# Optimization experiments

Measured on AMD Instinct MI355X. Metric: run time of the kernel, lower is better.

## Reference

```python
import jax, jax.numpy as jnp
import numpy as np

N = 100000      # nodes
E = 400000      # edges
G = 4096        # graphs in batch
ATOM_DIM = 101
BOND_DIM = 11
D = 128         # latent_dim
L = 3           # num_atom_layers
BN_EPS = 1e-5


def setup_inputs() -> dict:
    key = jax.random.key(0)
    ks = jax.random.split(key, 16)
    x = jax.random.normal(ks[0], (N, ATOM_DIM), dtype=jnp.float32)
    edge_index = jax.random.randint(ks[1], (2, E), 0, N, dtype=jnp.int64)
    batch = jnp.sort(jax.random.randint(ks[2], (N,), 0, G, dtype=jnp.int64))
    edge_attr = jax.random.normal(ks[3], (E, BOND_DIM), dtype=jnp.float32)
    s = 0.05
    embW = jax.random.normal(ks[4], (ATOM_DIM, D), dtype=jnp.float32) * s
    embB = jnp.zeros((D,), dtype=jnp.float32)
    bondW = jax.random.normal(ks[5], (L, BOND_DIM, D), dtype=jnp.float32) * s
    bondB = jnp.zeros((L, D), dtype=jnp.float32)
    W1 = jax.random.normal(ks[6], (L, D, 2 * D), dtype=jnp.float32) * s
    b1 = jnp.zeros((L, 2 * D), dtype=jnp.float32)
    g1 = jnp.ones((L, 2 * D), dtype=jnp.float32)
    be1 = jnp.zeros((L, 2 * D), dtype=jnp.float32)
    W2 = jax.random.normal(ks[7], (L, 2 * D, D), dtype=jnp.float32) * s
    b2 = jnp.zeros((L, D), dtype=jnp.float32)
    gout = jnp.ones((L, D), dtype=jnp.float32)
    bout = jnp.zeros((L, D), dtype=jnp.float32)
    return dict(x=x, edge_attr=edge_attr, embW=embW, embB=embB,
                bondW=bondW, bondB=bondB, W1=W1, b1=b1, g1=g1, be1=be1,
                W2=W2, b2=b2, gout=gout, bout=bout,
                edge_index=edge_index, batch=batch)


def _bn(h, gamma, beta):
    # BatchNorm1d in training mode: batch stats over node axis, biased variance
    m = h.mean(axis=0)
    v = h.var(axis=0)
    return (h - m) * jax.lax.rsqrt(v + BN_EPS) * gamma + beta


def reference(x, edge_attr, embW, embB, bondW, bondB, W1, b1, g1, be1,
              W2, b2, gout, bout, edge_index, batch):
    src, dst = edge_index[0], edge_index[1]
    h = x @ embW + embB                              # [N, D]
    for i in range(L):
        e = edge_attr @ bondW[i] + bondB[i]          # [E, D] bond embedding
        msg = jax.nn.relu(h[src] + e)                # gather + add + relu
        agg = jax.ops.segment_sum(msg, dst, num_segments=N)  # scatter-add
        z = h + agg                                  # (1 + eps) * x + agg, eps = 0
        z = jax.nn.relu(_bn(z @ W1[i] + b1[i], g1[i], be1[i]))  # [N, 2D]
        h = z @ W2[i] + b2[i]                        # [N, D]
        h = _bn(h, gout[i], bout[i])
        if i != L - 1:
            h = jax.nn.relu(h)
    # global mean pool per graph
    sums = jax.ops.segment_sum(h, batch, num_segments=G)            # [G, D]
    cnts = jax.ops.segment_sum(jnp.ones((h.shape[0],), h.dtype), batch,
                               num_segments=G)
    return sums / jnp.maximum(cnts, 1.0)[:, None]
```

## Files before the change

kernel.cpp:

```cpp
#include <hip/hip_runtime.h>
#include <hip/hip_bf16.h>

#define NN 100000
#define EE 400000
#define GG 4096
#define DD 128
#define ATOM_DIM 101
#define BOND_DIM 11
#define EAP 12
#define GEMM_GRID 512

typedef __attribute__((ext_vector_type(8))) short bf16x8;
typedef __attribute__((ext_vector_type(4))) float f32x4;
typedef __attribute__((ext_vector_type(2))) float f32x2;

__device__ __forceinline__ float b2f(short s) {
    unsigned u = ((unsigned)(unsigned short)s) << 16;
    float f; __builtin_memcpy(&f, &u, 4); return f;
}
__device__ __forceinline__ unsigned short f2b(float f) {
    unsigned u; __builtin_memcpy(&u, &f, 4);
    u += 0x7FFFu + ((u >> 16) & 1u);
    return (unsigned short)(u >> 16);
}

__global__ void detect64_kernel(const void* ei, int npairs, int* flag) {
    __shared__ int any;
    if (threadIdx.x == 0) any = 0;
    __syncthreads();
    const int* p = (const int*)ei;
    int v = 0;
    for (int i = threadIdx.x; i < npairs; i += blockDim.x) v |= p[2 * i + 1];
    if (v) atomicOr(&any, 1);
    __syncthreads();
    if (threadIdx.x == 0) *flag = (any == 0) ? 1 : 0;
}
__device__ __forceinline__ int getIdx(const void* p, long i, int is64) {
    if (is64) return (int)(((const long long*)p)[i]);
    return ((const int*)p)[i];
}

__global__ __launch_bounds__(256) void hist_kernel(
    const void* __restrict__ eidx, const int* __restrict__ flag, int* __restrict__ counts) {
    int e = blockIdx.x * 256 + threadIdx.x;
    if (e >= EE) return;
    int is64 = *flag;
    int dn = getIdx(eidx, (long)EE + e, is64);
    atomicAdd(&counts[dn], 1);
}

__global__ __launch_bounds__(256) void scan1_kernel(
    const int* __restrict__ counts, int* __restrict__ tmp, int* __restrict__ bsum, int n) {
    __shared__ int sd[256];
    const int tid = threadIdx.x;
    int i = blockIdx.x * 256 + tid;
    int v = (i < n) ? counts[i] : 0;
    sd[tid] = v; __syncthreads();
    #pragma unroll
    for (int off = 1; off < 256; off <<= 1) {
        int a = (tid >= off) ? sd[tid - off] : 0;
        __syncthreads();
        sd[tid] += a;
        __syncthreads();
    }
    if (i < n) tmp[i] = sd[tid] - v;
    if (tid == 255) bsum[blockIdx.x] = sd[255];
}

__global__ __launch_bounds__(512) void scan2_kernel(
    const int* __restrict__ bsum, int* __restrict__ bsumx, int nb) {
    __shared__ int sd[512];
    const int tid = threadIdx.x;
    int v = (tid < nb) ? bsum[tid] : 0;
    sd[tid] = v; __syncthreads();
    #pragma unroll
    for (int off = 1; off < 512; off <<= 1) {
        int a = (tid >= off) ? sd[tid - off] : 0;
        __syncthreads();
        sd[tid] += a;
        __syncthreads();
    }
    if (tid < nb) bsumx[tid] = sd[tid] - v;
}

__global__ __launch_bounds__(256) void scan3_kernel(
    const int* __restrict__ tmp, const int* __restrict__ bsumx,
    int* __restrict__ row_ptr, int n) {
    int i = blockIdx.x * 256 + threadIdx.x;
    if (i < n) row_ptr[i] = tmp[i] + bsumx[blockIdx.x];
    if (i == 0) row_ptr[n] = EE;
}

__global__ __launch_bounds__(256) void scatter_kernel(
    const void* __restrict__ eidx, const int* __restrict__ flag,
    const float* __restrict__ ea, const int* __restrict__ row_ptr,
    int* __restrict__ cursor, int* __restrict__ src_sorted, float* __restrict__ eas) {
    int e = blockIdx.x * 256 + threadIdx.x;
    if (e >= EE) return;
    int is64 = *flag;
    int dn = getIdx(eidx, (long)EE + e, is64);
    int sv = getIdx(eidx, e, is64);
    int pos = row_ptr[dn] + atomicAdd(&cursor[dn], 1);
    src_sorted[pos] = sv;
    const float* sp = ea + (long)e * BOND_DIM;
    float* dp = eas + (long)pos * EAP;
    #pragma unroll
    for (int k = 0; k < BOND_DIM; ++k) dp[k] = sp[k];
    dp[11] = 0.f;
}

#define EDGE_MATH(TV, EVp, A0, A1)                                              \
    {                                                                           \
        float c0 = bbv.x, c1 = bbv.y;                                           \
        _Pragma("unroll")                                                       \
        for (int k = 0; k < BOND_DIM; ++k) {                                    \
            c0 = fmaf((EVp)[k], wk0[k], c0);                                    \
            c1 = fmaf((EVp)[k], wk1[k], c1);                                    \
        }                                                                       \
        float f0 = b2f((short)((TV) & 0xffff)), f1 = b2f((short)((TV) >> 16));  \
        if (aff) { f0 = fmaxf(f0 * sc0 + sh0, 0.f); f1 = fmaxf(f1 * sc1v + sh1v, 0.f); } \
        A0 += fmaxf(f0 + c0, 0.f);                                              \
        A1 += fmaxf(f1 + c1, 0.f);                                              \
    }

__global__ __launch_bounds__(256) void msg_csr_kernel(
    const unsigned short* __restrict__ h,
    const float* __restrict__ sc, const float* __restrict__ sh,
    const int* __restrict__ src_sorted, const int* __restrict__ row_ptr,
    const float* __restrict__ eas,
    const float* __restrict__ bw,
    const float* __restrict__ bb,
    unsigned short* __restrict__ sout)
{
    const int tid = threadIdx.x;
    const int wave = tid >> 6, lane = tid & 63;
    const int d0 = lane * 2;
    float wk0[BOND_DIM], wk1[BOND_DIM];
    #pragma unroll
    for (int k = 0; k < BOND_DIM; ++k) {
        f32x2 wv = *(const f32x2*)(bw + k * DD + d0);
        wk0[k] = wv.x; wk1[k] = wv.y;
    }
    f32x2 bbv = *(const f32x2*)(bb + d0);
    const bool aff = (sc != nullptr);
    float sc0 = 1.f, sc1v = 1.f, sh0 = 0.f, sh1v = 0.f;
    if (aff) { sc0 = sc[d0]; sc1v = sc[d0 + 1]; sh0 = sh[d0]; sh1v = sh[d0 + 1]; }

    for (int n0 = blockIdx.x * 4 + wave; n0 < NN; n0 += gridDim.x * 4) {
        const int n = __builtin_amdgcn_readfirstlane(n0);
        const int e0 = __builtin_amdgcn_readfirstlane(row_ptr[n]);
        const int e1 = __builtin_amdgcn_readfirstlane(row_ptr[n + 1]);
        float a0 = 0.f, a1 = 0.f;
        int e = e0;
        for (; e + 4 <= e1; e += 4) {
            const int eu = __builtin_amdgcn_readfirstlane(e);
            int sv0 = __builtin_amdgcn_readfirstlane(src_sorted[eu]);
            int sv1 = __builtin_amdgcn_readfirstlane(src_sorted[eu + 1]);
            int sv2 = __builtin_amdgcn_readfirstlane(src_sorted[eu + 2]);
            int sv3 = __builtin_amdgcn_readfirstlane(src_sorted[eu + 3]);
            unsigned tv0 = *(const unsigned*)(h + (long)sv0 * DD + d0);
            unsigned tv1 = *(const unsigned*)(h + (long)sv1 * DD + d0);
            unsigned tv2 = *(const unsigned*)(h + (long)sv2 * DD + d0);
            unsigned tv3 = *(const unsigned*)(h + (long)sv3 * DD + d0);
            const float* ep0 = eas + (long)eu * EAP;
            EDGE_MATH(tv0, ep0, a0, a1)
            EDGE_MATH(tv1, ep0 + EAP, a0, a1)
            EDGE_MATH(tv2, ep0 + 2 * EAP, a0, a1)
            EDGE_MATH(tv3, ep0 + 3 * EAP, a0, a1)
        }
        if (e + 2 <= e1) {
            const int eu = __builtin_amdgcn_readfirstlane(e);
            int sv0 = __builtin_amdgcn_readfirstlane(src_sorted[eu]);
            int sv1 = __builtin_amdgcn_readfirstlane(src_sorted[eu + 1]);
            unsigned tv0 = *(const unsigned*)(h + (long)sv0 * DD + d0);
            unsigned tv1 = *(const unsigned*)(h + (long)sv1 * DD + d0);
            const float* ep0 = eas + (long)eu * EAP;
            EDGE_MATH(tv0, ep0, a0, a1)
            EDGE_MATH(tv1, ep0 + EAP, a0, a1)
            e += 2;
        }
        if (e < e1) {
            const int eu = __builtin_amdgcn_readfirstlane(e);
            int sv = __builtin_amdgcn_readfirstlane(src_sorted[eu]);
            unsigned tv = *(const unsigned*)(h + (long)sv * DD + d0);
            const float* ep0 = eas + (long)eu * EAP;
            EDGE_MATH(tv, ep0, a0, a1)
        }
        unsigned tn = *(const unsigned*)(h + (long)n * DD + d0);
        float t0 = b2f((short)(tn & 0xffff)), t1 = b2f((short)(tn >> 16));
        if (aff) {
            t0 = fmaxf(t0 * sc0 + sh0, 0.f); t1 = fmaxf(t1 * sc1v + sh1v, 0.f);
        }
        unsigned pk = (unsigned)f2b(t0 + a0) | ((unsigned)f2b(t1 + a1) << 16);
        *(unsigned*)(sout + (long)n * DD + d0) = pk;
    }
}

__global__ void pack_w(const float* __restrict__ W, unsigned short* __restrict__ Wf,
                       int Kact, int N, int KSTEPS) {
    int idx = blockIdx.x * blockDim.x + threadIdx.x;
    int NF = N >> 4;
    int total = KSTEPS * NF * 64;
    if (idx >= total) return;
    int l = idx & 63;
    int f = (idx >> 6) % NF;
    int ks = idx / (64 * NF);
    int col = f * 16 + (l & 15);
    int k0 = ks * 32 + (l >> 4) * 8;
    bf16x8 v;
    #pragma unroll
    for (int j = 0; j < 8; ++j) {
        int k = k0 + j;
        v[j] = (k < Kact) ? (short)f2b(W[(long)k * N + col]) : (short)0;
    }
    *(bf16x8*)(Wf + (long)idx * 8) = v;
}

template<int MODE, int KSTEPS, int KACT>
__device__ __forceinline__ void loadA(const void* Ap, long rc, int kg, bf16x8* dst) {
    if (MODE == 1) {
        const float* ap = (const float*)Ap + rc * KACT;
        #pragma unroll
        for (int ks = 0; ks < KSTEPS; ++ks) {
            bf16x8 a;
            #pragma unroll
            for (int j = 0; j < 8; ++j) {
                int gk = ks * 32 + kg + j;
                a[j] = (gk < KACT) ? (short)f2b(ap[gk]) : (short)0;
            }
            dst[ks] = a;
        }
    } else {
        const unsigned short* ap = (const unsigned short*)Ap + rc * (KSTEPS * 32) + kg;
        #pragma unroll
        for (int ks = 0; ks < KSTEPS; ++ks) dst[ks] = *(const bf16x8*)(ap + ks * 32);
    }
}

template<int NF, int KSTEPS, int NHALVES, int MODE, bool OUT_BF16, bool STATS, int KACT = 0>
__global__ __launch_bounds__(256, 2) void gemm_reg(
    const void* __restrict__ Ap,
    const float* __restrict__ sc, const float* __restrict__ sh,
    const unsigned short* __restrict__ Wf,
    const float* __restrict__ bias,
    void* __restrict__ outp,
    float* __restrict__ partial,
    int M)
{
    constexpr int K = KSTEPS * 32;
    constexpr int NCb = NF * 16;
    constexpr int NFtot = NF * NHALVES;
    constexpr int NCtot = NCb * NHALVES;
    constexpr int ESZ = OUT_BF16 ? 2 : 4;
    constexpr int RSTRIDE = NCb + (OUT_BF16 ? 8 : 4);
    constexpr int ROWBYTES = NCb * ESZ;
    constexpr int CHUNKS = 64 * ROWBYTES / 16;
    constexpr int CPR = ROWBYTES / 16;

    __shared__ __align__(16) char sOut[2][64 * RSTRIDE * ESZ];
    __shared__ float s_sc[(MODE == 2) ? K : 1];
    __shared__ float s_sh[(MODE == 2) ? K : 1];
    __shared__ float s_ps[STATS ? 2 * NCb : 1];

    const int tid = threadIdx.x;
    const int wave = tid >> 6, l = tid & 63;
    const int kg = (l >> 4) * 8;

    int half, mt;
    if (NHALVES == 2) {
        int b = blockIdx.x;
        half = (b >> 3) & 1;
        mt = (b & 7) | ((b >> 4) << 3);
    } else {
        half = 0; mt = blockIdx.x;
    }
    const int col0 = half * NCb;
    const int bstep = gridDim.x / NHALVES;

    if (MODE == 2 || STATS) {
        if (MODE == 2) {
            for (int i = tid; i < K; i += 256) { s_sc[i] = sc[i]; s_sh[i] = sh[i]; }
        }
        if (STATS) {
            for (int i = tid; i < 2 * NCb; i += 256) s_ps[i] = 0.f;
        }
        __syncthreads();
    }

    bf16x8 bfr[KSTEPS][NF];
    {
        const bf16x8* wp = (const bf16x8*)Wf;
        #pragma unroll
        for (int ks = 0; ks < KSTEPS; ++ks)
            #pragma unroll
            for (int f = 0; f < NF; ++f)
                bfr[ks][f] = wp[((long)ks * NFtot + half * NF + f) * 64 + l];
    }

    float bb[NF];
    #pragma unroll
    for (int f = 0; f < NF; ++f) bb[f] = bias[col0 + f * 16 + (l & 15)];

    float ssum[NF], ssq[NF];
    #pragma unroll
    for (int f = 0; f < NF; ++f) { ssum[f] = 0.f; ssq[f] = 0.f; }

    const int MT = (M + 63) >> 6;

    bf16x8 ldA[KSTEPS], ldB[KSTEPS];
    {
        int rr = mt * 64 + wave * 16 + (l & 15);
        int rc = rr < M ? rr : M - 1;
        loadA<MODE, KSTEPS, KACT>(Ap, rc, kg, ldA);
    }

    int pbuf = 0;
    for (; mt < MT; mt += bstep) {
        const int nxt = mt + bstep;
        if (nxt < MT) {
            int rr = nxt * 64 + wave * 16 + (l & 15);
            int rc = rr < M ? rr : M - 1;
            loadA<MODE, KSTEPS, KACT>(Ap, rc, kg, ldB);
        }

        if (MODE == 2) {
            #pragma unroll
            for (int ks = 0; ks < KSTEPS; ++ks) {
                f32x4 s0 = *(const f32x4*)&s_sc[ks * 32 + kg];
                f32x4 s1 = *(const f32x4*)&s_sc[ks * 32 + kg + 4];
                f32x4 h0 = *(const f32x4*)&s_sh[ks * 32 + kg];
                f32x4 h1 = *(const f32x4*)&s_sh[ks * 32 + kg + 4];
                float sv[8] = {s0.x, s0.y, s0.z, s0.w, s1.x, s1.y, s1.z, s1.w};
                float hv[8] = {h0.x, h0.y, h0.z, h0.w, h1.x, h1.y, h1.z, h1.w};
                #pragma unroll
                for (int j = 0; j < 8; ++j) {
                    float v = fmaxf(b2f(ldA[ks][j]) * sv[j] + hv[j], 0.f);
                    ldA[ks][j] = (short)f2b(v);
                }
            }
        }

        f32x4 acc[NF];
        #pragma unroll
        for (int f = 0; f < NF; ++f) acc[f] = (f32x4){0.f, 0.f, 0.f, 0.f};
        #pragma unroll
        for (int ks = 0; ks < KSTEPS; ++ks)
            #pragma unroll
            for (int f = 0; f < NF; ++f)
                acc[f] = __builtin_amdgcn_mfma_f32_16x16x32_bf16(ldA[ks], bfr[ks][f], acc[f], 0, 0, 0);

        const int rtile = mt * 64;
        char* sb = sOut[pbuf];
        #pragma unroll
        for (int f = 0; f < NF; ++f) {
            const int cl = f * 16 + (l & 15);
            #pragma unroll
            for (int j = 0; j < 4; ++j) {
                const int rl = wave * 16 + (l >> 4) * 4 + j;
                float v = acc[f][j] + bb[f];
                if (OUT_BF16) ((unsigned short*)sb)[rl * RSTRIDE + cl] = f2b(v);
                else          ((float*)sb)[rl * RSTRIDE + cl] = v;
                if (STATS && rtile + rl < M) { ssum[f] += v; ssq[f] += v * v; }
            }
        }
        __syncthreads();

        const int rmax = M - rtile;
        #pragma unroll
        for (int i = 0; i < CHUNKS / 256; ++i) {
            int c = i * 256 + tid;
            int row = c / CPR;
            int off = (c % CPR) * 16;
            if (row < rmax) {
                f32x4 v = *(const f32x4*)(sb + row * (RSTRIDE * ESZ) + off);
                char* gp = (char*)outp + ((long)(rtile + row) * NCtot + col0) * ESZ + off;
                *(f32x4*)gp = v;
            }
        }
        pbuf ^= 1;

        #pragma unroll
        for (int ks = 0; ks < KSTEPS; ++ks) ldA[ks] = ldB[ks];
    }

    if (STATS) {
        #pragma unroll
        for (int f = 0; f < NF; ++f) {
            float s = ssum[f], q = ssq[f];
            s += __shfl_xor(s, 16); s += __shfl_xor(s, 32);
            q += __shfl_xor(q, 16); q += __shfl_xor(q, 32);
            if (l < 16) {
                atomicAdd(&s_ps[f * 16 + l], s);
                atomicAdd(&s_ps[NCb + f * 16 + l], q);
            }
        }
        __syncthreads();
        float* pb = partial + (long)blockIdx.x * 2 * NCb;
        for (int i = tid; i < 2 * NCb; i += 256) pb[i] = s_ps[i];
    }
}

__global__ __launch_bounds__(64) void bn_finalize_p(
    const float* __restrict__ partial, int nblk, int ncb, int halves,
    const float* __restrict__ gamma, const float* __restrict__ beta,
    float invN, float* __restrict__ sc, float* __restrict__ sh)
{
    const int c = blockIdx.x;
    const int t = threadIdx.x;
    float s = 0.f, q = 0.f;
    for (int b = t; b < nblk; b += 64) {
        int half = (halves == 2) ? ((b >> 3) & 1) : 0;
        if (c / ncb != half) continue;
        const float* pb = partial + (long)b * 2 * ncb;
        s += pb[c % ncb];
        q += pb[ncb + c % ncb];
    }
    #pragma unroll
    for (int off = 1; off < 64; off <<= 1) {
        s += __shfl_xor(s, off);
        q += __shfl_xor(q, off);
    }
    if (t == 0) {
        float m = s * invN;
        float v = q * invN - m * m;
        float g = gamma[c] * rsqrtf(v + 1e-5f);
        sc[c] = g;
        sh[c] = beta[c] - m * g;
    }
}

__global__ __launch_bounds__(64) void pool_kernel(
    const unsigned short* __restrict__ h,
    const float* __restrict__ sc, const float* __restrict__ sh,
    const void* __restrict__ batchp, const int* __restrict__ flag,
    int Nn, float* __restrict__ out)
{
    const int g = blockIdx.x;
    const int t = threadIdx.x;
    const int d0 = t * 2;
    const int is64 = *flag;
    int lo = 0, hi = Nn;
    while (lo < hi) { int mid = (lo + hi) >> 1; if (getIdx(batchp, mid, is64) < g) lo = mid + 1; else hi = mid; }
    const int s0 = lo;
    hi = Nn;
    while (lo < hi) { int mid = (lo + hi) >> 1; if (getIdx(batchp, mid, is64) < g + 1) lo = mid + 1; else hi = mid; }
    const int s1 = lo;
    float a0 = 0.f, a1 = 0.f;
    for (int r = s0; r < s1; ++r) {
        unsigned v = *(const unsigned*)(h + (long)r * DD + d0);
        a0 += b2f((short)(v & 0xffff));
        a1 += b2f((short)(v >> 16));
    }
    const int cnt = s1 - s0;
    f32x2 o; o.x = 0.f; o.y = 0.f;
    if (cnt > 0) {
        float inv = 1.f / (float)cnt;
        o.x = a0 * inv * sc[d0] + sh[d0];
        o.y = a1 * inv * sc[d0 + 1] + sh[d0 + 1];
    }
    *(f32x2*)(out + (long)g * DD + d0) = o;
}

extern "C" void kernel_launch(void* const* d_in, const int* in_sizes, int n_in,
                              void* d_out, int out_size, void* d_ws, size_t ws_size,
                              hipStream_t stream)
{
    const float* x     = (const float*)d_in[0];
    const float* ea    = (const float*)d_in[1];
    const float* embW  = (const float*)d_in[2];
    const float* embB  = (const float*)d_in[3];
    const float* bondW = (const float*)d_in[4];
    const float* bondB = (const float*)d_in[5];
    const float* W1    = (const float*)d_in[6];
    const float* b1    = (const float*)d_in[7];
    const float* g1    = (const float*)d_in[8];
    const float* be1   = (const float*)d_in[9];
    const float* W2    = (const float*)d_in[10];
    const float* b2    = (const float*)d_in[11];
    const float* gout  = (const float*)d_in[12];
    const float* bout  = (const float*)d_in[13];
    const void*  eidx  = d_in[14];
    const void*  batch = d_in[15];
    float* out = (float*)d_out;

    char* w = (char*)d_ws;
    unsigned short* h   = (unsigned short*)w;   w += (long)NN * DD * 2;
    unsigned short* s   = (unsigned short*)w;   w += (long)NN * DD * 2;
    unsigned short* z1  = (unsigned short*)w;   w += (long)NN * 256 * 2;
    float* eas  = (float*)w;                    w += (long)EE * EAP * 4;
    int* src_sorted = (int*)w;                  w += (long)EE * 4;
    int* row_ptr    = (int*)w;                  w += (long)(NN + 1) * 4;
    int* counts     = (int*)w;                  w += (long)NN * 4;
    int* tmp        = (int*)w;                  w += (long)NN * 4;
    int* bsum       = (int*)w;                  w += 1024 * 4;
    int* bsumx      = (int*)w;                  w += 1024 * 4;
    float* partial  = (float*)w;                w += (long)GEMM_GRID * 512 * 4;
    float* sc1  = (float*)w;                    w += 256 * 4;
    float* sh1  = (float*)w;                    w += 256 * 4;
    float* sc2  = (float*)w;                    w += 128 * 4;
    float* sh2  = (float*)w;                    w += 128 * 4;
    unsigned short* embWf = (unsigned short*)w; w += 4 * 8  * 64 * 8 * 2;
    unsigned short* W1f   = (unsigned short*)w; w += 3L * 4 * 16 * 64 * 8 * 2;
    unsigned short* W2f   = (unsigned short*)w; w += 3L * 8 * 8  * 64 * 8 * 2;
    int* flag = (int*)w;

    detect64_kernel<<<1, 256, 0, stream>>>(eidx, 256, flag);

    pack_w<<<8, 256, 0, stream>>>(embW, embWf, ATOM_DIM, 128, 4);
    for (int i = 0; i < 3; ++i) {
        pack_w<<<16, 256, 0, stream>>>(W1 + (long)i * 128 * 256, W1f + (long)i * 4 * 16 * 64 * 8, 128, 256, 4);
        pack_w<<<16, 256, 0, stream>>>(W2 + (long)i * 256 * 128, W2f + (long)i * 8 * 8 * 64 * 8, 256, 128, 8);
    }

    const int eblocks = (EE + 255) / 256;
    const int nb = (NN + 255) / 256;
    hipMemsetAsync(counts, 0, (size_t)NN * 4, stream);
    hist_kernel<<<eblocks, 256, 0, stream>>>(eidx, flag, counts);
    scan1_kernel<<<nb, 256, 0, stream>>>(counts, tmp, bsum, NN);
    scan2_kernel<<<1, 512, 0, stream>>>(bsum, bsumx, nb);
    scan3_kernel<<<nb, 256, 0, stream>>>(tmp, bsumx, row_ptr, NN);
    hipMemsetAsync(counts, 0, (size_t)NN * 4, stream);
    scatter_kernel<<<eblocks, 256, 0, stream>>>(eidx, flag, ea, row_ptr, counts, src_sorted, eas);

    gemm_reg<8, 4, 1, 1, true, false, ATOM_DIM><<<GEMM_GRID, 256, 0, stream>>>(
        x, nullptr, nullptr, embWf, embB, h, nullptr, NN);

    const float* scin = nullptr;
    const float* shin = nullptr;

    for (int i = 0; i < 3; ++i) {
        msg_csr_kernel<<<4096, 256, 0, stream>>>(
            h, scin, shin, src_sorted, row_ptr, eas,
            bondW + (long)i * BOND_DIM * DD, bondB + (long)i * DD, s);

        gemm_reg<8, 4, 2, 0, true, true><<<GEMM_GRID, 256, 0, stream>>>(
            s, nullptr, nullptr, W1f + (long)i * 4 * 16 * 64 * 8,
            b1 + (long)i * 256, z1, partial, NN);
        bn_finalize_p<<<256, 64, 0, stream>>>(partial, GEMM_GRID, 128, 2,
            g1 + (long)i * 256, be1 + (long)i * 256, 1.f / NN, sc1, sh1);

        gemm_reg<4, 8, 2, 2, true, true><<<GEMM_GRID, 256, 0, stream>>>(
            z1, sc1, sh1, W2f + (long)i * 8 * 8 * 64 * 8,
            b2 + (long)i * DD, h, partial, NN);
        bn_finalize_p<<<128, 64, 0, stream>>>(partial, GEMM_GRID, 64, 2,
            gout + (long)i * DD, bout + (long)i * DD, 1.f / NN, sc2, sh2);

        scin = sc2; shin = sh2;
    }

    pool_kernel<<<GG, 64, 0, stream>>>(h, sc2, sh2, batch, flag, NN, out);
}
```

Baseline: 451.0 us.

## Fuse BN finalize into GEMM via last-block reduction and merge weight packing

Removes the separate bn_finalize_p launches by having the last GEMM block to finish (tracked with an atomic counter) reduce the per-block partial sums and write the BN scale and shift. All weight packing is merged into one pack_all kernel, and the two counter memsets become one by giving the scatter its own cursor array. This saves several kernel launches and their gaps. The cost is a serial tail where one block reads every partial, plus a dependence on a done counter that must reset itself between launches.

New measurement: 699.6 us. +55.1%, slower.

```diff
diff --git a/kernel.cpp b/kernel.cpp
--- a/kernel.cpp
+++ b/kernel.cpp
@@ -196,15 +196,27 @@
     }
 }
 
-__global__ void pack_w(const float* __restrict__ W, unsigned short* __restrict__ Wf,
-                       int Kact, int N, int KSTEPS) {
-    int idx = blockIdx.x * blockDim.x + threadIdx.x;
+__global__ __launch_bounds__(256) void pack_all(
+    const float* __restrict__ embW, const float* __restrict__ W1, const float* __restrict__ W2,
+    unsigned short* __restrict__ embWf, unsigned short* __restrict__ W1f, unsigned short* __restrict__ W2f)
+{
+    int idx = blockIdx.x * 256 + threadIdx.x;
+    const float* W; unsigned short* Wf; int Kact, N, base;
+    if (idx < 2048) {
+        W = embW; Wf = embWf; Kact = ATOM_DIM; N = 128; base = idx;
+    } else if (idx < 2048 + 3 * 4096) {
+        int r = idx - 2048; int i = r / 4096; base = r % 4096;
+        W = W1 + (long)i * 128 * 256; Wf = W1f + (long)i * 4096 * 8;
+        Kact = 128; N = 256;
+    } else if (idx < 2048 + 6 * 4096) {
+        int r = idx - 2048 - 3 * 4096; int i = r / 4096; base = r % 4096;
+        W = W2 + (long)i * 256 * 128; Wf = W2f + (long)i * 4096 * 8;
+        Kact = 256; N = 128;
+    } else return;
+    int l = base & 63;
     int NF = N >> 4;
-    int total = KSTEPS * NF * 64;
-    if (idx >= total) return;
-    int l = idx & 63;
-    int f = (idx >> 6) % NF;
-    int ks = idx / (64 * NF);
+    int f = (base >> 6) % NF;
+    int ks = base / (64 * NF);
     int col = f * 16 + (l & 15);
     int k0 = ks * 32 + (l >> 4) * 8;
     bf16x8 v;
@@ -213,7 +225,7 @@
         int k = k0 + j;
         v[j] = (k < Kact) ? (short)f2b(W[(long)k * N + col]) : (short)0;
     }
-    *(bf16x8*)(Wf + (long)idx * 8) = v;
+    *(bf16x8*)(Wf + (long)base * 8) = v;
 }
 
 template<int MODE, int KSTEPS, int KACT>
@@ -245,6 +257,9 @@
     const float* __restrict__ bias,
     void* __restrict__ outp,
     float* __restrict__ partial,
+    const float* __restrict__ gamma, const float* __restrict__ beta,
+    float* __restrict__ sc_out, float* __restrict__ sh_out,
+    int* __restrict__ done,
     int M)
 {
     constexpr int K = KSTEPS * 32;
@@ -261,6 +276,7 @@
     __shared__ float s_sc[(MODE == 2) ? K : 1];
     __shared__ float s_sh[(MODE == 2) ? K : 1];
     __shared__ float s_ps[STATS ? 2 * NCb : 1];
+    __shared__ int amLast;
 
     const int tid = threadIdx.x;
     const int wave = tid >> 6, l = tid & 63;
@@ -396,36 +412,37 @@
         }
         __syncthreads();
         float* pb = partial + (long)blockIdx.x * 2 * NCb;
-        for (int i = tid; i < 2 * NCb; i += 256) pb[i] = s_ps[i];
-    }
-}
-
-__global__ __launch_bounds__(64) void bn_finalize_p(
-    const float* __restrict__ partial, int nblk, int ncb, int halves,
-    const float* __restrict__ gamma, const float* __restrict__ beta,
-    float invN, float* __restrict__ sc, float* __restrict__ sh)
-{
-    const int c = blockIdx.x;
-    const int t = threadIdx.x;
-    float s = 0.f, q = 0.f;
-    for (int b = t; b < nblk; b += 64) {
-        int half = (halves == 2) ? ((b >> 3) & 1) : 0;
-        if (c / ncb != half) continue;
-        const float* pb = partial + (long)b * 2 * ncb;
-        s += pb[c % ncb];
-        q += pb[ncb + c % ncb];
-    }
-    #pragma unroll
-    for (int off = 1; off < 64; off <<= 1) {
-        s += __shfl_xor(s, off);
-        q += __shfl_xor(q, off);
-    }
-    if (t == 0) {
-        float m = s * invN;
-        float v = q * invN - m * m;
-        float g = gamma[c] * rsqrtf(v + 1e-5f);
-        sc[c] = g;
-        sh[c] = beta[c] - m * g;
+        for (int i = tid; i < 2 * NCb; i += 256)
+            __hip_atomic_store(&pb[i], s_ps[i], __ATOMIC_RELAXED, __HIP_MEMORY_SCOPE_AGENT);
+        __threadfence();
+        __syncthreads();
+        if (tid == 0) {
+            int prev = atomicAdd(done, 1);
+            amLast = (prev == (int)gridDim.x - 1);
+        }
+        __syncthreads();
+        if (amLast) {
+            __threadfence();
+            const float invN = 1.f / (float)M;
+            for (int c = tid; c < NCtot; c += 256) {
+                const int hh = c / NCb, cl = c % NCb;
+                float s = 0.f, q = 0.f;
+                const int nrel = (NHALVES == 2) ? (GEMM_GRID / 2) : GEMM_GRID;
+                #pragma unroll 8
+                for (int j = 0; j < nrel; ++j) {
+                    int b = (NHALVES == 2) ? (((j >> 3) << 4) | (hh << 3) | (j & 7)) : j;
+                    const float* pb2 = partial + (long)b * 2 * NCb;
+                    s += __hip_atomic_load(&pb2[cl], __ATOMIC_RELAXED, __HIP_MEMORY_SCOPE_AGENT);
+                    q += __hip_atomic_load(&pb2[NCb + cl], __ATOMIC_RELAXED, __HIP_MEMORY_SCOPE_AGENT);
+                }
+                float m = s * invN;
+                float v = q * invN - m * m;
+                float g = gamma[c] * rsqrtf(v + 1e-5f);
+                sc_out[c] = g;
+                sh_out[c] = beta[c] - m * g;
+            }
+            if (tid == 0) *done = 0;
+        }
     }
 }
 
@@ -491,6 +508,8 @@
     int* src_sorted = (int*)w;                  w += (long)EE * 4;
     int* row_ptr    = (int*)w;                  w += (long)(NN + 1) * 4;
     int* counts     = (int*)w;                  w += (long)NN * 4;
+    int* cursor     = (int*)w;                  w += (long)NN * 4;
+    int* done       = (int*)w;                  w += 16 * 4;
     int* tmp        = (int*)w;                  w += (long)NN * 4;
     int* bsum       = (int*)w;                  w += 1024 * 4;
     int* bsumx      = (int*)w;                  w += 1024 * 4;
@@ -504,26 +523,22 @@
     unsigned short* W2f   = (unsigned short*)w; w += 3L * 8 * 8  * 64 * 8 * 2;
     int* flag = (int*)w;
 
+    hipMemsetAsync(counts, 0, ((size_t)2 * NN + 16) * 4, stream);
+
     detect64_kernel<<<1, 256, 0, stream>>>(eidx, 256, flag);
-
-    pack_w<<<8, 256, 0, stream>>>(embW, embWf, ATOM_DIM, 128, 4);
-    for (int i = 0; i < 3; ++i) {
-        pack_w<<<16, 256, 0, stream>>>(W1 + (long)i * 128 * 256, W1f + (long)i * 4 * 16 * 64 * 8, 128, 256, 4);
-        pack_w<<<16, 256, 0, stream>>>(W2 + (long)i * 256 * 128, W2f + (long)i * 8 * 8 * 64 * 8, 256, 128, 8);
-    }
+    pack_all<<<(2048 + 6 * 4096 + 255) / 256, 256, 0, stream>>>(embW, W1, W2, embWf, W1f, W2f);
 
     const int eblocks = (EE + 255) / 256;
     const int nb = (NN + 255) / 256;
-    hipMemsetAsync(counts, 0, (size_t)NN * 4, stream);
     hist_kernel<<<eblocks, 256, 0, stream>>>(eidx, flag, counts);
     scan1_kernel<<<nb, 256, 0, stream>>>(counts, tmp, bsum, NN);
     scan2_kernel<<<1, 512, 0, stream>>>(bsum, bsumx, nb);
     scan3_kernel<<<nb, 256, 0, stream>>>(tmp, bsumx, row_ptr, NN);
-    hipMemsetAsync(counts, 0, (size_t)NN * 4, stream);
-    scatter_kernel<<<eblocks, 256, 0, stream>>>(eidx, flag, ea, row_ptr, counts, src_sorted, eas);
+    scatter_kernel<<<eblocks, 256, 0, stream>>>(eidx, flag, ea, row_ptr, cursor, src_sorted, eas);
 
     gemm_reg<8, 4, 1, 1, true, false, ATOM_DIM><<<GEMM_GRID, 256, 0, stream>>>(
-        x, nullptr, nullptr, embWf, embB, h, nullptr, NN);
+        x, nullptr, nullptr, embWf, embB, h, nullptr,
+        nullptr, nullptr, nullptr, nullptr, nullptr, NN);
 
     const float* scin = nullptr;
     const float* shin = nullptr;
@@ -535,15 +550,13 @@
 
         gemm_reg<8, 4, 2, 0, true, true><<<GEMM_GRID, 256, 0, stream>>>(
             s, nullptr, nullptr, W1f + (long)i * 4 * 16 * 64 * 8,
-            b1 + (long)i * 256, z1, partial, NN);
-        bn_finalize_p<<<256, 64, 0, stream>>>(partial, GEMM_GRID, 128, 2,
-            g1 + (long)i * 256, be1 + (long)i * 256, 1.f / NN, sc1, sh1);
+            b1 + (long)i * 256, z1, partial,
+            g1 + (long)i * 256, be1 + (long)i * 256, sc1, sh1, done, NN);
 
         gemm_reg<4, 8, 2, 2, true, true><<<GEMM_GRID, 256, 0, stream>>>(
             z1, sc1, sh1, W2f + (long)i * 8 * 8 * 64 * 8,
-            b2 + (long)i * DD, h, partial, NN);
-        bn_finalize_p<<<128, 64, 0, stream>>>(partial, GEMM_GRID, 64, 2,
-            gout + (long)i * DD, bout + (long)i * DD, 1.f / NN, sc2, sh2);
+            b2 + (long)i * DD, h, partial,
+            gout + (long)i * DD, bout + (long)i * DD, sc2, sh2, done, NN);
 
         scin = sc2; shin = sh2;
     }
```
